# Kernel tuning notes

Hardware: AMD Instinct MI355X
Metric: run time of the kernel (lower is better)

The kernel has to match this reference:

```python
import jax, jax.numpy as jnp
import numpy as np

NUM_HEADS = 16
WINDOW = 512
EPS = 1e-5


def layer_norm(x, g, b):
    m = jnp.mean(x, axis=-1, keepdims=True)
    v = jnp.var(x, axis=-1, keepdims=True)
    return (x - m) * jax.lax.rsqrt(v + EPS) * g + b


def rope(x, pos):
    # x: [B,H,S,D], rotate-half RoPE with base 10000
    D = x.shape[-1]
    inv_freq = 1.0 / (10000.0 ** (jnp.arange(0, D, 2, dtype=jnp.float32) / D))
    ang = pos[:, None].astype(jnp.float32) * inv_freq  # [S, D/2]
    cos = jnp.concatenate([jnp.cos(ang), jnp.cos(ang)], axis=-1)
    sin = jnp.concatenate([jnp.sin(ang), jnp.sin(ang)], axis=-1)
    x1, x2 = jnp.split(x, 2, axis=-1)
    rot = jnp.concatenate([-x2, x1], axis=-1)
    return x * cos + rot * sin


def setup_inputs() -> dict:
    key = jax.random.key(0)
    ks = jax.random.split(key, 8)
    B, S, Dm = 2, 2048, 1024
    Dff = 4 * Dm
    sc = 0.02
    return {
        'hidden_states': jax.random.normal(ks[0], (B, S, Dm), jnp.float32),
        'ln1_g': jnp.ones((Dm,), jnp.float32),
        'ln1_b': jnp.zeros((Dm,), jnp.float32),
        'wq': jax.random.normal(ks[1], (Dm, Dm), jnp.float32) * sc,
        'bq': jnp.zeros((Dm,), jnp.float32),
        'wk': jax.random.normal(ks[2], (Dm, Dm), jnp.float32) * sc,
        'bk': jnp.zeros((Dm,), jnp.float32),
        'wv': jax.random.normal(ks[3], (Dm, Dm), jnp.float32) * sc,
        'bv': jnp.zeros((Dm,), jnp.float32),
        'wo': jax.random.normal(ks[4], (Dm, Dm), jnp.float32) * sc,
        'bo': jnp.zeros((Dm,), jnp.float32),
        'ln2_g': jnp.ones((Dm,), jnp.float32),
        'ln2_b': jnp.zeros((Dm,), jnp.float32),
        'w1': jax.random.normal(ks[5], (Dm, Dff), jnp.float32) * sc,
        'b1': jnp.zeros((Dff,), jnp.float32),
        'w2': jax.random.normal(ks[6], (Dff, Dm), jnp.float32) * sc,
        'b2': jnp.zeros((Dm,), jnp.float32),
        'global_token_indices': jax.random.randint(ks[7], (8,), 0, S, jnp.int32),
    }


def reference(hidden_states, ln1_g, ln1_b, wq, bq, wk, bk, wv, bv, wo, bo,
              ln2_g, ln2_b, w1, b1, w2, b2, global_token_indices):
    B, S, Dm = hidden_states.shape
    H = NUM_HEADS
    Dh = Dm // H

    # --- attention block ---
    x = layer_norm(hidden_states, ln1_g, ln1_b)
    heads = lambda t: t.reshape(B, S, H, Dh).transpose(0, 2, 1, 3)  # [B,H,S,Dh]
    q = heads(x @ wq + bq)
    k = heads(x @ wk + bk)
    v = heads(x @ wv + bv)

    pos = jnp.arange(S)
    q = rope(q, pos)
    k = rope(k, pos)

    scores = jnp.einsum('bhqd,bhkd->bhqk', q, k) / jnp.sqrt(jnp.float32(Dh))
    i = pos[:, None]
    j = pos[None, :]
    causal = j <= i
    band = causal & ((i - j) < WINDOW)
    is_global = jnp.zeros((S,), bool).at[global_token_indices].set(True)
    allowed = band | (causal & (is_global[None, :] | is_global[:, None]))
    scores = jnp.where(allowed[None, None], scores, jnp.float32(-1e9))
    attn = jax.nn.softmax(scores, axis=-1)
    ctx = jnp.einsum('bhqk,bhkd->bhqd', attn, v)
    ctx = ctx.transpose(0, 2, 1, 3).reshape(B, S, Dm)
    attn_out = ctx @ wo + bo
    h = hidden_states + attn_out

    # --- MLP block ---
    y = layer_norm(h, ln2_g, ln2_b)
    mlp = jax.nn.gelu(y @ w1 + b1, approximate=False) @ w2 + b2
    return h + mlp
```

## Files before the change

kernel.cpp:

```cpp
#include <hip/hip_runtime.h>

typedef unsigned short u16;
typedef __bf16 bf16x8 __attribute__((ext_vector_type(8)));
typedef short s16x8 __attribute__((ext_vector_type(8)));
typedef float f32x4 __attribute__((ext_vector_type(4)));

#define NB 2
#define SS 2048
#define DM 1024
#define NH 16
#define DH 64
#define DFF 4096

__device__ __forceinline__ u16 f2bf(float f) {
    unsigned u = __float_as_uint(f);
    u += 0x7fff + ((u >> 16) & 1);
    return (u16)(u >> 16);
}
__device__ __forceinline__ float bf2f(u16 h) {
    return __uint_as_float(((unsigned)h) << 16);
}
__device__ __forceinline__ void gld_lds16(const void* g, void* l) {
    __builtin_amdgcn_global_load_lds(
        (const __attribute__((address_space(1))) unsigned int*)(size_t)g,
        (__attribute__((address_space(3))) unsigned int*)(unsigned)(size_t)l,
        16, 0, 0);
}
__device__ __forceinline__ float gelu_f(float x) {
    return 0.5f * x * (1.f + erff(x * 0.70710678118654752f));
}

__global__ void wtrans_kernel(const float* __restrict__ w, u16* __restrict__ wt,
                              int K, int N) {
    __shared__ unsigned tl[64][65];
    int n0 = blockIdx.x * 64, k0 = blockIdx.y * 64, t = threadIdx.x;
    for (int it = 0; it < 16; ++it) {
        int e = it * 256 + t; int r = e >> 6, c = e & 63;
        tl[r][c] = f2bf(w[(size_t)(k0 + r) * N + n0 + c]);
    }
    __syncthreads();
    for (int it = 0; it < 16; ++it) {
        int e = it * 256 + t; int r = e >> 6, c = e & 63;
        wt[(size_t)(n0 + r) * K + k0 + c] = (u16)tl[c][r];
    }
}

__global__ void wtrans4_kernel(const float* __restrict__ a, const float* __restrict__ b,
                               const float* __restrict__ c, const float* __restrict__ d,
                               u16* __restrict__ oa, u16* __restrict__ ob,
                               u16* __restrict__ oc, u16* __restrict__ od) {
    __shared__ unsigned tl[64][65];
    const float* w; u16* wt;
    switch (blockIdx.z) {
        case 0: w = a; wt = oa; break;
        case 1: w = b; wt = ob; break;
        case 2: w = c; wt = oc; break;
        default: w = d; wt = od; break;
    }
    int n0 = blockIdx.x * 64, k0 = blockIdx.y * 64, t = threadIdx.x;
    for (int it = 0; it < 16; ++it) {
        int e = it * 256 + t; int r = e >> 6, cc = e & 63;
        tl[r][cc] = f2bf(w[(size_t)(k0 + r) * DM + n0 + cc]);
    }
    __syncthreads();
    for (int it = 0; it < 16; ++it) {
        int e = it * 256 + t; int r = e >> 6, cc = e & 63;
        wt[(size_t)(n0 + r) * DM + k0 + cc] = (u16)tl[cc][r];
    }
}

__global__ void build_aux(const int* __restrict__ gti, unsigned long long* __restrict__ kmask,
                          const float* __restrict__ bq, const float* __restrict__ bk,
                          const float* __restrict__ bv, float* __restrict__ bias3) {
    int t = threadIdx.x;
    if (t < 32) {
        unsigned long long m = 0ull;
        #pragma unroll
        for (int i = 0; i < 8; ++i) {
            int g = gti[i];
            if ((g >> 6) == t) m |= 1ull << (g & 63);
        }
        kmask[t] = m;
    }
    for (int i = t; i < 1024; i += 256) {
        bias3[i] = bq[i]; bias3[1024 + i] = bk[i]; bias3[2048 + i] = bv[i];
    }
}

template <bool INIT>
__global__ __launch_bounds__(256) void ln_kernel(const float* __restrict__ x,
                                                 const float* __restrict__ g,
                                                 const float* __restrict__ b,
                                                 u16* __restrict__ out,
                                                 const float* __restrict__ ib,
                                                 float* __restrict__ iout) {
    int row = blockIdx.x, t = threadIdx.x;
    const float4 v = ((const float4*)(x + (size_t)row * DM))[t];
    float s  = v.x + v.y + v.z + v.w;
    float sq = v.x * v.x + v.y * v.y + v.z * v.z + v.w * v.w;
    #pragma unroll
    for (int m = 1; m < 64; m <<= 1) { s += __shfl_xor(s, m); sq += __shfl_xor(sq, m); }
    __shared__ float ss[4], ssq[4];
    int wv = t >> 6, lane = t & 63;
    if (lane == 0) { ss[wv] = s; ssq[wv] = sq; }
    __syncthreads();
    s  = ss[0] + ss[1] + ss[2] + ss[3];
    sq = ssq[0] + ssq[1] + ssq[2] + ssq[3];
    float mean = s * (1.f / DM);
    float var  = sq * (1.f / DM) - mean * mean;
    float rs   = rsqrtf(var + 1e-5f);
    float4 gg = ((const float4*)g)[t];
    float4 bb = ((const float4*)b)[t];
    ushort4 o;
    o.x = f2bf((v.x - mean) * rs * gg.x + bb.x);
    o.y = f2bf((v.y - mean) * rs * gg.y + bb.y);
    o.z = f2bf((v.z - mean) * rs * gg.z + bb.z);
    o.w = f2bf((v.w - mean) * rs * gg.w + bb.w);
    ((ushort4*)(out + (size_t)row * DM))[t] = o;
    if (INIT) {
        float4 b2 = ((const float4*)ib)[t];
        float4 iv; iv.x = v.x + b2.x; iv.y = v.y + b2.y; iv.z = v.z + b2.z; iv.w = v.w + b2.w;
        ((float4*)(iout + (size_t)row * DM))[t] = iv;
    }
}

__global__ __launch_bounds__(256) void rope_kernel(const u16* __restrict__ qkv,
                                                   u16* __restrict__ qh,
                                                   u16* __restrict__ kh) {
    int idx = blockIdx.x * 256 + threadIdx.x;
    int d = idx & 31;
    int s = (idx >> 5) & (SS - 1);
    int h = (idx >> 16) & (NH - 1);
    int b = idx >> 20;
    size_t src = ((size_t)(b * SS + s)) * 3072 + h * DH + d;
    size_t dst = ((size_t)((b * NH + h) * SS + s)) * DH + d;
    float inv = powf(10000.f, -(float)d * (1.f / 32.f));
    float ang = (float)s * inv;
    float sn, cs;
    sincosf(ang, &sn, &cs);
    const float QSC = 0.125f;
    float x1 = bf2f(qkv[src]), x2 = bf2f(qkv[src + 32]);
    qh[dst]      = f2bf((x1 * cs - x2 * sn) * QSC);
    qh[dst + 32] = f2bf((x2 * cs + x1 * sn) * QSC);
    x1 = bf2f(qkv[src + 1024]); x2 = bf2f(qkv[src + 1024 + 32]);
    kh[dst]      = f2bf(x1 * cs - x2 * sn);
    kh[dst + 32] = f2bf(x2 * cs + x1 * sn);
}

__global__ __launch_bounds__(256) void vtrans_kernel(const u16* __restrict__ qkv,
                                                     u16* __restrict__ vt) {
    __shared__ unsigned tile[64][65];
    int st = blockIdx.x, bh = blockIdx.y;
    int b = bh >> 4, h = bh & 15, t = threadIdx.x;
    const u16* src = qkv + ((size_t)b * SS + st * 64) * 3072 + 2048 + h * DH;
    for (int it = 0; it < 16; ++it) {
        int e = it * 256 + t; int r = e >> 6, c = e & 63;
        tile[r][c] = src[(size_t)r * 3072 + c];
    }
    __syncthreads();
    u16* dst = vt + ((size_t)bh * DH) * SS + st * 64;
    for (int it = 0; it < 16; ++it) {
        int e = it * 256 + t; int d = e >> 6, s = e & 63;
        dst[(size_t)d * SS + s] = (u16)tile[s][d];
    }
}

template <int MODE>
__global__ __launch_bounds__(256) void gemm_bt(const u16* __restrict__ A,
                                               const u16* __restrict__ Bt,
                                               const float* __restrict__ bias,
                                               const float* __restrict__ res,
                                               void* __restrict__ Cout,
                                               int M, int N, int K, int ldk) {
    const int bm = blockIdx.y * 128, bn = blockIdx.x * 128;
    const int koff = blockIdx.z * K;
    const int t = threadIdx.x, wv = t >> 6, lane = t & 63;
    const int lr = lane & 15, lq = lane >> 4;
    const int wm = (wv >> 1) * 64, wn = (wv & 1) * 64;
    __shared__ __align__(16) u16 As[2][128 * 64];
    __shared__ __align__(16) u16 Bs[2][128 * 64];
    f32x4 acc[4][4] = {};

    auto stage = [&](int kb, int buf) {
        #pragma unroll
        for (int p = 0; p < 4; ++p) {
            int c = p * 256 + t;
            int r = c >> 3;
            int gc = ((c & 7) ^ (r & 7)) * 8;
            gld_lds16(A + (size_t)(bm + r) * ldk + kb + gc,
                      As[buf] + (size_t)(p * 256 + wv * 64) * 8);
            gld_lds16(Bt + (size_t)(bn + r) * ldk + kb + gc,
                      Bs[buf] + (size_t)(p * 256 + wv * 64) * 8);
        }
    };

    stage(koff, 0);
    int pb = 0;
    for (int k0 = 0; k0 < K; k0 += 64) {
        __syncthreads();
        if (k0 + 64 < K) stage(koff + k0 + 64, pb ^ 1);
        const u16* Ac = As[pb];
        const u16* Bc = Bs[pb];
        #pragma unroll
        for (int ks = 0; ks < 2; ++ks) {
            bf16x8 af[4], bfr[4];
            #pragma unroll
            for (int mi = 0; mi < 4; ++mi) {
                int row = wm + mi * 16 + lr;
                af[mi] = *(const bf16x8*)&Ac[row * 64 + (((ks * 4 + lq) ^ (row & 7)) * 8)];
            }
            #pragma unroll
            for (int ni = 0; ni < 4; ++ni) {
                int row = wn + ni * 16 + lr;
                bfr[ni] = *(const bf16x8*)&Bs[pb][row * 64 + (((ks * 4 + lq) ^ (row & 7)) * 8)];
            }
            #pragma unroll
            for (int mi = 0; mi < 4; ++mi)
                #pragma unroll
                for (int ni = 0; ni < 4; ++ni)
                    acc[mi][ni] = __builtin_amdgcn_mfma_f32_16x16x32_bf16(af[mi], bfr[ni], acc[mi][ni], 0, 0, 0);
        }
        pb ^= 1;
    }
    #pragma unroll
    for (int mi = 0; mi < 4; ++mi) {
        int row0 = bm + wm + mi * 16 + lq * 4;
        #pragma unroll
        for (int ni = 0; ni < 4; ++ni) {
            int col = bn + wn + ni * 16 + lr;
            float bv = (MODE == 3) ? 0.f : bias[col];
            #pragma unroll
            for (int r = 0; r < 4; ++r) {
                float v = acc[mi][ni][r] + bv;
                size_t off = (size_t)(row0 + r) * N + col;
                if (MODE == 1) v += res[off];
                if (MODE == 2) v = gelu_f(v);
                if (MODE == 0 || MODE == 2) ((u16*)Cout)[off] = f2bf(v);
                else if (MODE == 1)         ((float*)Cout)[off] = v;
                else                        atomicAdd((float*)Cout + off, v);
            }
        }
    }
}

template <int MODE>
__global__ __launch_bounds__(512, 2) void gemm256(const u16* __restrict__ A,
                                                  const u16* __restrict__ Bt,
                                                  const float* __restrict__ bias,
                                                  void* __restrict__ Cout,
                                                  int M, int N, int K, int ldk) {
    const int bm = blockIdx.y * 256, bn = blockIdx.x * 256;
    const int t = threadIdx.x, wv = t >> 6, lane = t & 63;
    const int lr = lane & 15, lq = lane >> 4;
    const int wm = (wv >> 2) * 128, wn = (wv & 3) * 64;
    const int awb = (wv >> 2) * 64;
    const int bwb = (wv & 3) * 32;
    __shared__ __align__(16) u16 As[2 * 2 * 128 * 64];
    __shared__ __align__(16) u16 Bs[2 * 2 * 128 * 64];
    f32x4 acc[8][4] = {};
    bf16x8 aA[4][2], bA[2][2], bB[2][2];

    const u16 *pAsrc[2][2], *pBsrc[2][2];
    #pragma unroll
    for (int g = 0; g < 2; ++g)
        #pragma unroll
        for (int p = 0; p < 2; ++p) {
            int c = p * 512 + t;
            int glr = c >> 3, sl = c & 7;
            int sc = (sl ^ (glr & 7)) * 8;
            int grA = (glr & 63) + g * 64 + ((glr >> 6) << 7);
            int grB = (glr & 31) + g * 32 + ((glr >> 5) << 6);
            pAsrc[g][p] = A  + (size_t)(bm + grA) * ldk + sc;
            pBsrc[g][p] = Bt + (size_t)(bn + grB) * ldk + sc;
        }
    auto AsP = [&](int db, int g) { return As + (size_t)(db * 2 + g) * 8192; };
    auto BsP = [&](int db, int g) { return Bs + (size_t)(db * 2 + g) * 8192; };
    auto stA = [&](int g, int db, int ku) {
        #pragma unroll
        for (int p = 0; p < 2; ++p)
            gld_lds16(pAsrc[g][p] + ku, AsP(db, g) + (size_t)(p * 512 + wv * 64) * 8);
    };
    auto stB = [&](int g, int db, int ku) {
        #pragma unroll
        for (int p = 0; p < 2; ++p)
            gld_lds16(pBsrc[g][p] + ku, BsP(db, g) + (size_t)(p * 512 + wv * 64) * 8);
    };
    auto loadA = [&](const u16* base) {
        #pragma unroll
        for (int mi2 = 0; mi2 < 4; ++mi2)
            #pragma unroll
            for (int ks = 0; ks < 2; ++ks) {
                int glr = awb + mi2 * 16 + lr;
                aA[mi2][ks] = *(const bf16x8*)&base[glr * 64 + (((ks * 4 + lq) ^ (glr & 7)) * 8)];
            }
    };
    auto loadB = [&](const u16* base, bf16x8 (&dst)[2][2]) {
        #pragma unroll
        for (int ni2 = 0; ni2 < 2; ++ni2)
            #pragma unroll
            for (int ks = 0; ks < 2; ++ks) {
                int glr = bwb + ni2 * 16 + lr;
                dst[ni2][ks] = *(const bf16x8*)&base[glr * 64 + (((ks * 4 + lq) ^ (glr & 7)) * 8)];
            }
    };
    auto mmac = [&](int qm, int qn, bf16x8 (&bb)[2][2]) {
        __builtin_amdgcn_s_setprio(1);
        #pragma unroll
        for (int mi2 = 0; mi2 < 4; ++mi2)
            #pragma unroll
            for (int ni2 = 0; ni2 < 2; ++ni2)
                #pragma unroll
                for (int ks = 0; ks < 2; ++ks)
                    acc[qm * 4 + mi2][qn * 2 + ni2] =
                        __builtin_amdgcn_mfma_f32_16x16x32_bf16(
                            aA[mi2][ks], bb[ni2][ks], acc[qm * 4 + mi2][qn * 2 + ni2], 0, 0, 0);
        __builtin_amdgcn_s_setprio(0);
    };
    #define LGKM0_FENCE  do { asm volatile("s_waitcnt lgkmcnt(0)" ::: "memory"); \
                              __builtin_amdgcn_sched_barrier(0); } while (0)

    const int NT = K >> 6;
    stA(0, 0, 0); stA(1, 0, 0); stB(0, 0, 0); stB(1, 0, 0);
    asm volatile("s_waitcnt vmcnt(2)" ::: "memory");
    __builtin_amdgcn_s_barrier();

    for (int kt = 0; kt < NT - 1; ++kt) {
        const int db = kt & 1, nb2 = db ^ 1;
        const int ku = (kt + 1) * 64;
        loadA(AsP(db, 0)); loadB(BsP(db, 0), bA);
        stA(0, nb2, ku);
        __builtin_amdgcn_s_barrier();
        LGKM0_FENCE;
        mmac(0, 0, bA);
        asm volatile("s_waitcnt vmcnt(2)" ::: "memory");
        __builtin_amdgcn_s_barrier();
        loadB(BsP(db, 1), bB);
        stA(1, nb2, ku);
        __builtin_amdgcn_s_barrier();
        LGKM0_FENCE;
        mmac(0, 1, bB);
        __builtin_amdgcn_s_barrier();
        loadA(AsP(db, 1));
        stB(0, nb2, ku);
        __builtin_amdgcn_s_barrier();
        LGKM0_FENCE;
        mmac(1, 1, bB);
        __builtin_amdgcn_s_barrier();
        stB(1, nb2, ku);
        __builtin_amdgcn_s_barrier();
        LGKM0_FENCE;
        mmac(1, 0, bA);
        asm volatile("s_waitcnt vmcnt(2)" ::: "memory");
        __builtin_amdgcn_s_barrier();
    }
    {
        const int db = (NT - 1) & 1;
        loadA(AsP(db, 0)); loadB(BsP(db, 0), bA);
        __builtin_amdgcn_s_barrier();
        LGKM0_FENCE;
        mmac(0, 0, bA);
        asm volatile("s_waitcnt vmcnt(0)" ::: "memory");
        __builtin_amdgcn_s_barrier();
        loadB(BsP(db, 1), bB);
        __builtin_amdgcn_s_barrier();
        LGKM0_FENCE;
        mmac(0, 1, bB);
        __builtin_amdgcn_s_barrier();
        loadA(AsP(db, 1));
        __builtin_amdgcn_s_barrier();
        LGKM0_FENCE;
        mmac(1, 1, bB);
        mmac(1, 0, bA);
    }
    #undef LGKM0_FENCE

    #pragma unroll
    for (int mi = 0; mi < 8; ++mi) {
        int row0 = bm + wm + mi * 16 + lq * 4;
        #pragma unroll
        for (int ni = 0; ni < 4; ++ni) {
            int col = bn + wn + ni * 16 + lr;
            float bv = bias[col];
            #pragma unroll
            for (int r = 0; r < 4; ++r) {
                float v = acc[mi][ni][r] + bv;
                size_t off = (size_t)(row0 + r) * N + col;
                if (MODE == 2) v = gelu_f(v);
                ((u16*)Cout)[off] = f2bf(v);
            }
        }
    }
}

__global__ __launch_bounds__(256) void attn_kernel(const u16* __restrict__ qh,
                                                   const u16* __restrict__ kh,
                                                   const u16* __restrict__ vt,
                                                   const unsigned long long* __restrict__ kmask,
                                                   u16* __restrict__ ctx) {
    const int qt = blockIdx.x, bh = blockIdx.y;
    const int b = bh >> 4, h = bh & 15;
    const int t = threadIdx.x, wv = t >> 6, lane = t & 63;
    const int lr = lane & 15, lq = lane >> 4;
    const int q0 = qt * 64;

    __shared__ __align__(16) u16 Qs[64 * 64];
    __shared__ __align__(16) u16 Ks[2][64 * 64];
    __shared__ __align__(16) u16 Vs[2][64 * 64];
    __shared__ __align__(16) u16 Ps[64 * 64];

    const u16* qbase = qh + ((size_t)bh * SS) * DH;
    const u16* kbase = kh + ((size_t)bh * SS) * DH;
    const u16* vbase = vt + ((size_t)bh * DH) * SS;

    #pragma unroll
    for (int p = 0; p < 2; ++p) {
        int c = p * 256 + t; int r = c >> 3, sl = c & 7;
        gld_lds16(qbase + (size_t)(q0 + r) * DH + ((sl ^ (r & 7)) * 8),
                  Qs + (size_t)(p * 256 + wv * 64) * 8);
    }

    float sum_part[4] = {0.f, 0.f, 0.f, 0.f};
    f32x4 acc_o[4] = {};

    const int lim = qt - 8;
    int cur = 0;
    while (cur < lim && kmask[cur] == 0ull) ++cur;
    {
        int k0 = cur * 64;
        #pragma unroll
        for (int p = 0; p < 2; ++p) {
            int c = p * 256 + t; int r = c >> 3; int gc = ((c & 7) ^ (r & 7)) * 8;
            gld_lds16(kbase + (size_t)(k0 + r) * DH + gc, Ks[0] + (size_t)(p * 256 + wv * 64) * 8);
            gld_lds16(vbase + (size_t)r * SS + k0 + gc,  Vs[0] + (size_t)(p * 256 + wv * 64) * 8);
        }
    }
    int pb = 0;
    while (cur >= 0) {
        int nxt = cur + 1;
        while (nxt < lim && kmask[nxt] == 0ull) ++nxt;
        if (nxt > qt) nxt = -1;
        __syncthreads();
        if (nxt >= 0) {
            int k0n = nxt * 64;
            #pragma unroll
            for (int p = 0; p < 2; ++p) {
                int c = p * 256 + t; int r = c >> 3; int gc = ((c & 7) ^ (r & 7)) * 8;
                gld_lds16(kbase + (size_t)(k0n + r) * DH + gc, Ks[pb ^ 1] + (size_t)(p * 256 + wv * 64) * 8);
                gld_lds16(vbase + (size_t)r * SS + k0n + gc,  Vs[pb ^ 1] + (size_t)(p * 256 + wv * 64) * 8);
            }
        }
        const u16* Kt = Ks[pb];
        const u16* Vt = Vs[pb];
        const int k0 = cur * 64;

        f32x4 s_acc[4] = {};
        #pragma unroll
        for (int ks = 0; ks < 2; ++ks) {
            const int arow = wv * 16 + lr;
            bf16x8 af = *(const bf16x8*)&Qs[arow * 64 + (((ks * 4 + lq) ^ (arow & 7)) * 8)];
            #pragma unroll
            for (int ni = 0; ni < 4; ++ni) {
                const int brow = ni * 16 + lr;
                bf16x8 bfr = *(const bf16x8*)&Kt[brow * 64 + (((ks * 4 + lq) ^ (brow & 7)) * 8)];
                s_acc[ni] = __builtin_amdgcn_mfma_f32_16x16x32_bf16(af, bfr, s_acc[ni], 0, 0, 0);
            }
        }
        float sv[4][4];
        if (cur >= qt - 7 && cur != qt) {
            #pragma unroll
            for (int ni = 0; ni < 4; ++ni)
                #pragma unroll
                for (int r = 0; r < 4; ++r) sv[ni][r] = __expf(s_acc[ni][r]);
        } else if (cur == qt) {
            #pragma unroll
            for (int ni = 0; ni < 4; ++ni) {
                int j = ni * 16 + lr;
                #pragma unroll
                for (int r = 0; r < 4; ++r) {
                    int i = wv * 16 + lq * 4 + r;
                    float p = __expf(s_acc[ni][r]);
                    sv[ni][r] = (j <= i) ? p : 0.f;
                }
            }
        } else {
            unsigned long long cm = kmask[cur];
            #pragma unroll
            for (int ni = 0; ni < 4; ++ni) {
                int j = k0 + ni * 16 + lr;
                bool gj = (cm >> (ni * 16 + lr)) & 1ull;
                #pragma unroll
                for (int r = 0; r < 4; ++r) {
                    int i = q0 + wv * 16 + lq * 4 + r;
                    bool ok = ((i - j) < 512) | gj;
                    float p = __expf(s_acc[ni][r]);
                    sv[ni][r] = ok ? p : 0.f;
                }
            }
        }
        #pragma unroll
        for (int ni = 0; ni < 4; ++ni) {
            int col = ni * 16 + lr;
            #pragma unroll
            for (int r = 0; r < 4; ++r) {
                int row = wv * 16 + lq * 4 + r;
                sum_part[r] += sv[ni][r];
                Ps[row * 64 + (((col >> 3) ^ (row & 7)) * 8) + (col & 7)] = f2bf(sv[ni][r]);
            }
        }
        #pragma unroll
        for (int ks = 0; ks < 2; ++ks) {
            const int arow = wv * 16 + lr;
            bf16x8 af = *(const bf16x8*)&Ps[arow * 64 + (((ks * 4 + lq) ^ (arow & 7)) * 8)];
            #pragma unroll
            for (int ni = 0; ni < 4; ++ni) {
                const int brow = ni * 16 + lr;
                bf16x8 bfr = *(const bf16x8*)&Vt[brow * 64 + (((ks * 4 + lq) ^ (brow & 7)) * 8)];
                acc_o[ni] = __builtin_amdgcn_mfma_f32_16x16x32_bf16(af, bfr, acc_o[ni], 0, 0, 0);
            }
        }
        cur = nxt; pb ^= 1;
    }
    float inv_l[4];
    #pragma unroll
    for (int r = 0; r < 4; ++r) {
        float ls = sum_part[r];
        #pragma unroll
        for (int m = 1; m < 16; m <<= 1) ls += __shfl_xor(ls, m, 16);
        inv_l[r] = 1.f / ls;
    }
    u16* obase = ctx + ((size_t)b * SS) * DM + h * DH;
    #pragma unroll
    for (int ni = 0; ni < 4; ++ni)
        #pragma unroll
        for (int r = 0; r < 4; ++r) {
            int i = q0 + wv * 16 + lq * 4 + r;
            obase[(size_t)i * DM + ni * 16 + lr] = f2bf(acc_o[ni][r] * inv_l[r]);
        }
}

__global__ __launch_bounds__(256) void attn_fix_kernel(const u16* __restrict__ qh,
                                                       const u16* __restrict__ kh,
                                                       const u16* __restrict__ qkv,
                                                       const int* __restrict__ gti,
                                                       u16* __restrict__ ctx) {
    const int gidx = blockIdx.x, bh = blockIdx.y;
    const int b = bh >> 4, h = bh & 15;
    const int t = threadIdx.x, wv = t >> 6, lane = t & 63;
    const int i = gti[gidx];

    __shared__ float qsh[64];
    if (t < 64) qsh[t] = bf2f(qh[((size_t)bh * SS + i) * DH + t]);
    __syncthreads();
    float qreg[64];
    #pragma unroll
    for (int c = 0; c < 16; ++c) {
        float4 qv = ((const float4*)qsh)[c];
        qreg[c * 4 + 0] = qv.x; qreg[c * 4 + 1] = qv.y;
        qreg[c * 4 + 2] = qv.z; qreg[c * 4 + 3] = qv.w;
    }

    const u16* kb = kh + (size_t)bh * SS * DH;
    const u16* vb = qkv + (size_t)b * SS * 3072 + 2048 + h * DH;

    float Oacc[64];
    #pragma unroll
    for (int d = 0; d < 64; ++d) Oacc[d] = 0.f;
    float lacc = 0.f;

    for (int j0 = wv * 64; j0 <= i; j0 += 256) {
        const int j = j0 + lane;
        const bool valid = (j <= i);
        const int jc = valid ? j : i;
        const s16x8* krow = (const s16x8*)(kb + (size_t)jc * DH);
        float part[8];
        #pragma unroll
        for (int c = 0; c < 8; ++c) {
            s16x8 kv = krow[c];
            float p0 = 0.f;
            #pragma unroll
            for (int e = 0; e < 8; ++e) p0 += qreg[c * 8 + e] * bf2f((u16)kv[e]);
            part[c] = p0;
        }
        float s = ((part[0] + part[1]) + (part[2] + part[3])) +
                  ((part[4] + part[5]) + (part[6] + part[7]));
        const float p = valid ? __expf(s) : 0.f;
        lacc += p;
        const s16x8* vrow = (const s16x8*)(vb + (size_t)jc * 3072);
        #pragma unroll
        for (int c = 0; c < 8; ++c) {
            s16x8 vv = vrow[c];
            #pragma unroll
            for (int e = 0; e < 8; ++e) Oacc[c * 8 + e] += p * bf2f((u16)vv[e]);
        }
    }
    #pragma unroll
    for (int m = 1; m < 64; m <<= 1) {
        lacc += __shfl_xor(lacc, m);
        #pragma unroll
        for (int d = 0; d < 64; ++d) Oacc[d] += __shfl_xor(Oacc[d], m);
    }
    float out = 0.f;
    #pragma unroll
    for (int d = 0; d < 64; ++d) out = (lane == d) ? Oacc[d] : out;
    __shared__ float osum[4][64];
    __shared__ float lsum[4];
    osum[wv][lane] = out;
    if (lane == 0) lsum[wv] = lacc;
    __syncthreads();
    if (wv == 0) {
        float ot = osum[0][lane] + osum[1][lane] + osum[2][lane] + osum[3][lane];
        float lt = lsum[0] + lsum[1] + lsum[2] + lsum[3];
        ctx[((size_t)b * SS + i) * DM + h * DH + lane] = f2bf(ot / lt);
    }
}

extern "C" void kernel_launch(void* const* d_in, const int* in_sizes, int n_in,
                              void* d_out, int out_size, void* d_ws, size_t ws_size,
                              hipStream_t stream) {
    (void)in_sizes; (void)n_in; (void)out_size; (void)ws_size;
    const float* hidden = (const float*)d_in[0];
    const float* ln1_g  = (const float*)d_in[1];
    const float* ln1_b  = (const float*)d_in[2];
    const float* wq = (const float*)d_in[3];  const float* bq = (const float*)d_in[4];
    const float* wk = (const float*)d_in[5];  const float* bk = (const float*)d_in[6];
    const float* wv = (const float*)d_in[7];  const float* bv = (const float*)d_in[8];
    const float* wo = (const float*)d_in[9];  const float* bo = (const float*)d_in[10];
    const float* ln2_g = (const float*)d_in[11];
    const float* ln2_b = (const float*)d_in[12];
    const float* w1 = (const float*)d_in[13]; const float* b1 = (const float*)d_in[14];
    const float* w2 = (const float*)d_in[15]; const float* b2 = (const float*)d_in[16];
    const int*  gti = (const int*)d_in[17];

    char* ws = (char*)d_ws;
    const size_t MB = 1u << 20;
    u16* wqt  = (u16*)(ws + 0 * MB);
    u16* wkt  = (u16*)(ws + 2 * MB);
    u16* wvt  = (u16*)(ws + 4 * MB);
    u16* wot  = (u16*)(ws + 6 * MB);
    u16* w1t  = (u16*)(ws + 8 * MB);
    u16* w2t  = (u16*)(ws + 16 * MB);
    u16* xb   = (u16*)(ws + 24 * MB);
    u16* ctx  = xb;
    u16* qkv  = (u16*)(ws + 32 * MB);
    u16* qhb  = (u16*)(ws + 56 * MB);
    u16* khb  = (u16*)(ws + 64 * MB);
    u16* vtb  = (u16*)(ws + 72 * MB);
    float* hb = (float*)(ws + 80 * MB);
    u16* act  = (u16*)(ws + 32 * MB);
    u16* yb   = (u16*)(ws + 64 * MB);
    unsigned long long* kmask = (unsigned long long*)(ws + 96 * MB);
    float* bias3 = (float*)(ws + 96 * MB + 8192);

    wtrans4_kernel<<<dim3(16, 16, 4), 256, 0, stream>>>(wq, wk, wv, wo, wqt, wkt, wvt, wot);
    wtrans_kernel<<<dim3(64, 16), 256, 0, stream>>>(w1, w1t, DM, DFF);
    wtrans_kernel<<<dim3(16, 64), 256, 0, stream>>>(w2, w2t, DFF, DM);
    build_aux<<<1, 256, 0, stream>>>(gti, kmask, bq, bk, bv, bias3);

    ln_kernel<false><<<NB * SS, 256, 0, stream>>>(hidden, ln1_g, ln1_b, xb, nullptr, nullptr);

    gemm256<0><<<dim3(3072 / 256, (NB * SS) / 256), 512, 0, stream>>>(
        xb, wqt, bias3, qkv, NB * SS, 3072, DM, DM);

    rope_kernel<<<(NB * NH * SS * 32) / 256, 256, 0, stream>>>(qkv, qhb, khb);
    vtrans_kernel<<<dim3(SS / 64, NB * NH), 256, 0, stream>>>(qkv, vtb);

    attn_kernel<<<dim3(SS / 64, NB * NH), 256, 0, stream>>>(qhb, khb, vtb, kmask, ctx);
    attn_fix_kernel<<<dim3(8, NB * NH), 256, 0, stream>>>(qhb, khb, qkv, gti, ctx);

    gemm_bt<1><<<dim3(8, 32), 256, 0, stream>>>(ctx, wot, bo, hidden, hb, NB * SS, DM, DM, DM);
    ln_kernel<true><<<NB * SS, 256, 0, stream>>>(hb, ln2_g, ln2_b, yb, b2, (float*)d_out);
    gemm256<2><<<dim3(DFF / 256, (NB * SS) / 256), 512, 0, stream>>>(
        yb, w1t, b1, act, NB * SS, DFF, DM, DM);
    gemm_bt<3><<<dim3(8, 32, 2), 256, 0, stream>>>(act, w2t, nullptr, nullptr, d_out, NB * SS, DM, DFF / 2, DFF);
}
```

Before: 397.1 us.

## Remap GEMM blocks across XCDs and deepen gemm256 prefetch pipeline

Adds an XCD-aware block-index remap to both GEMM kernels. Each of the 8 XCDs gets a contiguous band of M rows, so tiles that share an A panel hit the same L2. It also restructures the gemm256 main loop to issue global-to-LDS loads up to two k-steps ahead, with adjusted vmcnt waits and a peeled second-to-last iteration. The intent is more L2 reuse and better hiding of memory latency behind MFMA work. The risks are extra index arithmetic and subtle LDS buffer hazards from writing into the buffer currently being read.

```diff
diff --git a/kernel.cpp b/kernel.cpp
--- a/kernel.cpp
+++ b/kernel.cpp
@@ -165,15 +165,27 @@
     }
 }
 
-template <int MODE>
+__device__ __forceinline__ void xcd_remap(int& bn, int& bm, int& bz) {
+    int s = blockIdx.x + gridDim.x * (blockIdx.y + gridDim.y * blockIdx.z);
+    int q = gridDim.y >> 3;
+    int xcd = s & 7, lin = s >> 3;
+    bm = xcd * q + (lin % q);
+    int rest = lin / q;
+    bn = rest % gridDim.x;
+    bz = rest / gridDim.x;
+}
+
+template <int MODE, int REMAP>
 __global__ __launch_bounds__(256) void gemm_bt(const u16* __restrict__ A,
                                                const u16* __restrict__ Bt,
                                                const float* __restrict__ bias,
                                                const float* __restrict__ res,
                                                void* __restrict__ Cout,
                                                int M, int N, int K, int ldk) {
-    const int bm = blockIdx.y * 128, bn = blockIdx.x * 128;
-    const int koff = blockIdx.z * K;
+    int bnb = blockIdx.x, bmb = blockIdx.y, bzb = blockIdx.z;
+    if (REMAP) xcd_remap(bnb, bmb, bzb);
+    const int bm = bmb * 128, bn = bnb * 128;
+    const int koff = bzb * K;
     const int t = threadIdx.x, wv = t >> 6, lane = t & 63;
     const int lr = lane & 15, lq = lane >> 4;
     const int wm = (wv >> 1) * 64, wn = (wv & 1) * 64;
@@ -212,7 +224,7 @@
             #pragma unroll
             for (int ni = 0; ni < 4; ++ni) {
                 int row = wn + ni * 16 + lr;
-                bfr[ni] = *(const bf16x8*)&Bs[pb][row * 64 + (((ks * 4 + lq) ^ (row & 7)) * 8)];
+                bfr[ni] = *(const bf16x8*)&Bc[row * 64 + (((ks * 4 + lq) ^ (row & 7)) * 8)];
             }
             #pragma unroll
             for (int mi = 0; mi < 4; ++mi)
@@ -243,13 +255,15 @@
     }
 }
 
-template <int MODE>
+template <int MODE, int REMAP>
 __global__ __launch_bounds__(512, 2) void gemm256(const u16* __restrict__ A,
                                                   const u16* __restrict__ Bt,
                                                   const float* __restrict__ bias,
                                                   void* __restrict__ Cout,
                                                   int M, int N, int K, int ldk) {
-    const int bm = blockIdx.y * 256, bn = blockIdx.x * 256;
+    int bnb = blockIdx.x, bmb = blockIdx.y, bzb = blockIdx.z;
+    if (REMAP) xcd_remap(bnb, bmb, bzb);
+    const int bm = bmb * 256, bn = bnb * 256;
     const int t = threadIdx.x, wv = t >> 6, lane = t & 63;
     const int lr = lane & 15, lq = lane >> 4;
     const int wm = (wv >> 2) * 128, wn = (wv & 3) * 64;
@@ -316,63 +330,83 @@
                             aA[mi2][ks], bb[ni2][ks], acc[qm * 4 + mi2][qn * 2 + ni2], 0, 0, 0);
         __builtin_amdgcn_s_setprio(0);
     };
-    #define LGKM0_FENCE  do { asm volatile("s_waitcnt lgkmcnt(0)" ::: "memory"); \
-                              __builtin_amdgcn_sched_barrier(0); } while (0)
+    #define BAR       __builtin_amdgcn_s_barrier()
+    #define LGKM0     do { asm volatile("s_waitcnt lgkmcnt(0)" ::: "memory"); \
+                           __builtin_amdgcn_sched_barrier(0); } while (0)
+    #define VMW(n)    asm volatile("s_waitcnt vmcnt(" #n ")" ::: "memory")
 
     const int NT = K >> 6;
-    stA(0, 0, 0); stA(1, 0, 0); stB(0, 0, 0); stB(1, 0, 0);
-    asm volatile("s_waitcnt vmcnt(2)" ::: "memory");
-    __builtin_amdgcn_s_barrier();
-
-    for (int kt = 0; kt < NT - 1; ++kt) {
-        const int db = kt & 1, nb2 = db ^ 1;
-        const int ku = (kt + 1) * 64;
+    stA(0, 0, 0); stB(0, 0, 0); stA(1, 0, 0); stB(1, 0, 0);
+    stA(0, 1, 64); stB(0, 1, 64);
+    VMW(8);
+    BAR;
+
+    for (int kt = 0; kt <= NT - 3; ++kt) {
+        const int db = kt & 1, nx = db ^ 1;
+        const int ku1 = (kt + 1) << 6, ku2 = (kt + 2) << 6;
         loadA(AsP(db, 0)); loadB(BsP(db, 0), bA);
-        stA(0, nb2, ku);
-        __builtin_amdgcn_s_barrier();
-        LGKM0_FENCE;
+        stA(1, nx, ku1);
+        BAR; LGKM0;
         mmac(0, 0, bA);
-        asm volatile("s_waitcnt vmcnt(2)" ::: "memory");
-        __builtin_amdgcn_s_barrier();
+        VMW(6);
+        BAR;
         loadB(BsP(db, 1), bB);
-        stA(1, nb2, ku);
-        __builtin_amdgcn_s_barrier();
-        LGKM0_FENCE;
+        stB(1, nx, ku1);
+        BAR; LGKM0;
         mmac(0, 1, bB);
-        __builtin_amdgcn_s_barrier();
+        BAR;
         loadA(AsP(db, 1));
-        stB(0, nb2, ku);
-        __builtin_amdgcn_s_barrier();
-        LGKM0_FENCE;
+        stA(0, db, ku2);
+        BAR; LGKM0;
         mmac(1, 1, bB);
-        __builtin_amdgcn_s_barrier();
-        stB(1, nb2, ku);
-        __builtin_amdgcn_s_barrier();
-        LGKM0_FENCE;
+        BAR;
+        stB(0, db, ku2);
+        BAR;
         mmac(1, 0, bA);
-        asm volatile("s_waitcnt vmcnt(2)" ::: "memory");
-        __builtin_amdgcn_s_barrier();
+        VMW(8);
+        BAR;
+    }
+    {
+        const int db = (NT - 2) & 1, nx = db ^ 1;
+        const int ku1 = (NT - 1) << 6;
+        loadA(AsP(db, 0)); loadB(BsP(db, 0), bA);
+        stA(1, nx, ku1);
+        BAR; LGKM0;
+        mmac(0, 0, bA);
+        VMW(6);
+        BAR;
+        loadB(BsP(db, 1), bB);
+        stB(1, nx, ku1);
+        BAR; LGKM0;
+        mmac(0, 1, bB);
+        BAR;
+        loadA(AsP(db, 1));
+        BAR; LGKM0;
+        mmac(1, 1, bB);
+        BAR;
+        mmac(1, 0, bA);
+        VMW(4);
+        BAR;
     }
     {
         const int db = (NT - 1) & 1;
         loadA(AsP(db, 0)); loadB(BsP(db, 0), bA);
-        __builtin_amdgcn_s_barrier();
-        LGKM0_FENCE;
+        BAR; LGKM0;
         mmac(0, 0, bA);
-        asm volatile("s_waitcnt vmcnt(0)" ::: "memory");
-        __builtin_amdgcn_s_barrier();
+        VMW(0);
+        BAR;
         loadB(BsP(db, 1), bB);
-        __builtin_amdgcn_s_barrier();
-        LGKM0_FENCE;
+        BAR; LGKM0;
         mmac(0, 1, bB);
-        __builtin_amdgcn_s_barrier();
+        BAR;
         loadA(AsP(db, 1));
-        __builtin_amdgcn_s_barrier();
-        LGKM0_FENCE;
+        BAR; LGKM0;
         mmac(1, 1, bB);
         mmac(1, 0, bA);
     }
-    #undef LGKM0_FENCE
+    #undef BAR
+    #undef LGKM0
+    #undef VMW
 
     #pragma unroll
     for (int mi = 0; mi < 8; ++mi) {
@@ -658,7 +692,7 @@
 
     ln_kernel<false><<<NB * SS, 256, 0, stream>>>(hidden, ln1_g, ln1_b, xb, nullptr, nullptr);
 
-    gemm256<0><<<dim3(3072 / 256, (NB * SS) / 256), 512, 0, stream>>>(
+    gemm256<0, 1><<<dim3(3072 / 256, (NB * SS) / 256), 512, 0, stream>>>(
         xb, wqt, bias3, qkv, NB * SS, 3072, DM, DM);
 
     rope_kernel<<<(NB * NH * SS * 32) / 256, 256, 0, stream>>>(qkv, qhb, khb);
@@ -667,9 +701,9 @@
     attn_kernel<<<dim3(SS / 64, NB * NH), 256, 0, stream>>>(qhb, khb, vtb, kmask, ctx);
     attn_fix_kernel<<<dim3(8, NB * NH), 256, 0, stream>>>(qhb, khb, qkv, gti, ctx);
 
-    gemm_bt<1><<<dim3(8, 32), 256, 0, stream>>>(ctx, wot, bo, hidden, hb, NB * SS, DM, DM, DM);
+    gemm_bt<1, 1><<<dim3(8, 32), 256, 0, stream>>>(ctx, wot, bo, hidden, hb, NB * SS, DM, DM, DM);
     ln_kernel<true><<<NB * SS, 256, 0, stream>>>(hb, ln2_g, ln2_b, yb, b2, (float*)d_out);
-    gemm256<2><<<dim3(DFF / 256, (NB * SS) / 256), 512, 0, stream>>>(
+    gemm256<2, 1><<<dim3(DFF / 256, (NB * SS) / 256), 512, 0, stream>>>(
         yb, w1t, b1, act, NB * SS, DFF, DM, DM);
-    gemm_bt<3><<<dim3(8, 32, 2), 256, 0, stream>>>(act, w2t, nullptr, nullptr, d_out, NB * SS, DM, DFF / 2, DFF);
-}
+    gemm_bt<3, 1><<<dim3(8, 32, 2), 256, 0, stream>>>(act, w2t, nullptr, nullptr, d_out, NB * SS, DM, DFF / 2, DFF);
+}
```

Result: faster. 386.0 us (-2.8%).
